# Kernel tuning notes

Measured on AMD Instinct MI355X. Metric: run time of the kernel, lower is better.

## Reference

```python
import jax, jax.numpy as jnp
import numpy as np

NUM_EMBEDDINGS = 1024
EMBEDDING_DIM = 256


def setup_inputs() -> dict:
    key = jax.random.key(0)
    k1, k2 = jax.random.split(key)
    z = jax.random.normal(k1, (32, EMBEDDING_DIM, 32, 32), dtype=jnp.float32)
    codebook = jax.random.normal(k2, (NUM_EMBEDDINGS, EMBEDDING_DIM), dtype=jnp.float32)
    return {"z": z, "codebook": codebook}


def reference(z, codebook):
    # z: (B, C, H, W) -> (B, H, W, C) -> (B*H*W, C)
    B, C, H, W = z.shape
    z_bhwc = jnp.transpose(z, (0, 2, 3, 1))
    z_flat = z_bhwc.reshape(-1, C)  # (N, C)

    # pairwise squared distances: ||z||^2 + ||e||^2 - 2 z.e^T  -> (N, K)
    distances = (
        jnp.sum(z_flat ** 2, axis=1, keepdims=True)
        + jnp.sum(codebook ** 2, axis=1)
        - 2.0 * jnp.matmul(z_flat, codebook.T)
    )
    argmin_codewords = jnp.argmin(distances, axis=1)  # (N,)
    min_codewords = jax.nn.one_hot(argmin_codewords, NUM_EMBEDDINGS, dtype=jnp.float32)  # (N, K)

    # quantized latents via one-hot @ codebook, back to (B, C, H, W)
    z_quantized = jnp.matmul(min_codewords, codebook).reshape(B, H, W, C)
    z_quantized = jnp.transpose(z_quantized, (0, 3, 1, 2))
    return (min_codewords, z_quantized)
```

## Files before the change

kernel.cpp:

```cpp
#include <hip/hip_runtime.h>

#define N_ROWS 32768
#define K_CODES 1024
#define CDIM 256

typedef _Float16 half8 __attribute__((ext_vector_type(8)));
typedef _Float16 half4 __attribute__((ext_vector_type(4)));
typedef float floatx16 __attribute__((ext_vector_type(16)));
typedef unsigned long long ull;

#define WS_ZH   0ull
#define WS_ZL   16777216ull
#define WS_CBH  33554432ull
#define WS_CBL  34078720ull
#define WS_CBN  34603008ull
#define WS_PART 34607104ull
#define WS_IDX  36704256ull
#define WS_NEED 36835328ull

__device__ __forceinline__ void g2lds16(const void* g, void* l) {
    __builtin_amdgcn_global_load_lds(
        (const __attribute__((address_space(1))) void*)g,
        (__attribute__((address_space(3))) void*)l, 16, 0, 0);
}

__global__ __launch_bounds__(256) void prep_all(const float* __restrict__ z,
                                                const float* __restrict__ cb,
                                                _Float16* __restrict__ zh,
                                                _Float16* __restrict__ zl,
                                                _Float16* __restrict__ cbh,
                                                _Float16* __restrict__ cbl,
                                                float* __restrict__ cbn) {
    __shared__ float t[64][68];
    if (blockIdx.x >= 2048) {
        int k = ((blockIdx.x - 2048) << 2) | (threadIdx.x >> 6);
        int lane = threadIdx.x & 63;
        float4 v = reinterpret_cast<const float4*>(cb + k * CDIM)[lane];
        float s0 = v.x * 32.f, s1 = v.y * 32.f, s2 = v.z * 32.f, s3 = v.w * 32.f;
        half4 hv, lv;
        hv[0] = (_Float16)s0; lv[0] = (_Float16)(s0 - (float)hv[0]);
        hv[1] = (_Float16)s1; lv[1] = (_Float16)(s1 - (float)hv[1]);
        hv[2] = (_Float16)s2; lv[2] = (_Float16)(s2 - (float)hv[2]);
        hv[3] = (_Float16)s3; lv[3] = (_Float16)(s3 - (float)hv[3]);
        size_t off = (size_t)((lane >> 3) * K_CODES + k) * 32 + ((lane * 4) & 31);
        *reinterpret_cast<half4*>(&cbh[off]) = hv;
        *reinterpret_cast<half4*>(&cbl[off]) = lv;
        float s = s0 * s0 + s1 * s1 + s2 * s2 + s3 * s3;
        #pragma unroll
        for (int off2 = 32; off2 > 0; off2 >>= 1) s += __shfl_down(s, off2);
        if (lane == 0) cbn[k] = s;
        return;
    }
    int hwt = blockIdx.x & 15;
    int ct  = (blockIdx.x >> 4) & 3;
    int bb  = blockIdx.x >> 6;
    int tid = threadIdx.x;
    #pragma unroll
    for (int p = 0; p < 4; p++) {
        int e = p * 256 + tid;
        int c = e >> 4, h4 = e & 15;
        float4 v = *reinterpret_cast<const float4*>(
            &z[((bb * 256 + ct * 64 + c) << 10) + hwt * 64 + h4 * 4]);
        *reinterpret_cast<float4*>(&t[c][h4 * 4]) = v;
    }
    __syncthreads();
    #pragma unroll
    for (int p = 0; p < 4; p++) {
        int e = p * 256 + tid;
        int hw = e >> 4, c4 = e & 15;
        half4 hv, lv;
        #pragma unroll
        for (int j = 0; j < 4; j++) {
            float s = t[c4 * 4 + j][hw] * 32.f;
            _Float16 h = (_Float16)s;
            hv[j] = h;
            lv[j] = (_Float16)(s - (float)h);
        }
        int n = bb * 1024 + hwt * 64 + hw;
        int cg = ct * 64 + c4 * 4;
        size_t off = (size_t)((cg >> 5) * N_ROWS + n) * 32 + (cg & 31);
        *reinterpret_cast<half4*>(&zh[off]) = hv;
        *reinterpret_cast<half4*>(&zl[off]) = lv;
    }
}

__global__ __launch_bounds__(256, 2) void vq_mfma32(
    const _Float16* __restrict__ zh, const _Float16* __restrict__ zl,
    const _Float16* __restrict__ cbh, const _Float16* __restrict__ cbl,
    const float* __restrict__ cbn, ull* __restrict__ partial) {

    __shared__ _Float16 AhL[2][4096], AlL[2][4096];
    __shared__ _Float16 BhL[2][4096], BlL[2][4096];
    __shared__ float rvv[128][2];
    __shared__ int   rcc[128][2];

    const int tid = threadIdx.x;
    const int lane = tid & 63, wave = tid >> 6;
    const int wm = wave & 1, wn = wave >> 1;
    const int fm = lane & 31, fq = lane >> 5;
    const int codeTile = blockIdx.x & 7;
    const int rowTile  = blockIdx.x >> 3;
    const int rowBase = rowTile * 128, codeBase = codeTile * 128;

    floatx16 acc[4];
    #pragma unroll
    for (int i = 0; i < 4; i++) acc[i] = (floatx16)0.f;

    auto stage = [&](int buf, int ch) {
        const size_t ab = (size_t)(ch * N_ROWS + rowBase) * 32;
        const size_t bbo = (size_t)(ch * K_CODES + codeBase) * 32;
        #pragma unroll
        for (int i = 0; i < 2; i++) {
            int G = i * 256 + tid;
            int q = G >> 7, r = G & 127;
            size_t so = (size_t)r * 32 + q * 8;
            g2lds16(zh + ab + so,  &AhL[buf][G * 8]);
            g2lds16(zl + ab + so,  &AlL[buf][G * 8]);
            g2lds16(cbh + bbo + so, &BhL[buf][G * 8]);
            g2lds16(cbl + bbo + so, &BlL[buf][G * 8]);
        }
    };

    stage(0, 0);
    for (int c = 0; c < 8; c++) {
        const int cur = c & 1;
        if (c < 7) {
            stage(cur ^ 1, c + 1);
            asm volatile("s_waitcnt vmcnt(8)" ::: "memory");
        } else {
            asm volatile("s_waitcnt vmcnt(0)" ::: "memory");
        }
        __builtin_amdgcn_s_barrier();
        #pragma unroll
        for (int s = 0; s < 2; s++) {
            int q = s * 2 + fq;
            half8 ah[2], al[2], bh[2], bl[2];
            #pragma unroll
            for (int i = 0; i < 2; i++) {
                int ga = q * 128 + wm * 64 + i * 32 + fm;
                ah[i] = *reinterpret_cast<const half8*>(&AhL[cur][ga * 8]);
                al[i] = *reinterpret_cast<const half8*>(&AlL[cur][ga * 8]);
            }
            #pragma unroll
            for (int j = 0; j < 2; j++) {
                int gb = q * 128 + wn * 64 + j * 32 + fm;
                bh[j] = *reinterpret_cast<const half8*>(&BhL[cur][gb * 8]);
                bl[j] = *reinterpret_cast<const half8*>(&BlL[cur][gb * 8]);
            }
            #pragma unroll
            for (int i = 0; i < 2; i++)
                #pragma unroll
                for (int j = 0; j < 2; j++) {
                    acc[i*2+j] = __builtin_amdgcn_mfma_f32_32x32x16_f16(ah[i], bh[j], acc[i*2+j], 0, 0, 0);
                    acc[i*2+j] = __builtin_amdgcn_mfma_f32_32x32x16_f16(al[i], bh[j], acc[i*2+j], 0, 0, 0);
                    acc[i*2+j] = __builtin_amdgcn_mfma_f32_32x32x16_f16(ah[i], bl[j], acc[i*2+j], 0, 0, 0);
                }
        }
        __builtin_amdgcn_s_barrier();
    }

    float cbnv[2];
    #pragma unroll
    for (int j = 0; j < 2; j++) cbnv[j] = cbn[codeBase + wn * 64 + j * 32 + fm];

    #pragma unroll
    for (int i = 0; i < 2; i++)
        #pragma unroll
        for (int r = 0; r < 16; r++) {
            float best = 3.4e38f; int bcode = 0x7fffffff;
            #pragma unroll
            for (int j = 0; j < 2; j++) {
                float d = fmaf(-2.f, acc[i*2+j][r], cbnv[j]);
                int code = codeBase + wn * 64 + j * 32 + fm;
                if (d < best) { best = d; bcode = code; }
            }
            #pragma unroll
            for (int m = 1; m < 32; m <<= 1) {
                float ov = __shfl_xor(best, m, 64);
                int   oc = __shfl_xor(bcode, m, 64);
                if (ov < best || (ov == best && oc < bcode)) { best = ov; bcode = oc; }
            }
            if (fm == 0) {
                int row = wm * 64 + i * 32 + (r & 3) + 8 * (r >> 2) + 4 * fq;
                rvv[row][wn] = best;
                rcc[row][wn] = bcode;
            }
        }
    __syncthreads();
    if (tid < 128) {
        float v0 = rvv[tid][0]; int c0 = rcc[tid][0];
        float v1 = rvv[tid][1]; int c1 = rcc[tid][1];
        if (v1 < v0 || (v1 == v0 && c1 < c0)) { v0 = v1; c0 = c1; }
        unsigned u = __float_as_uint(v0);
        u = (u & 0x80000000u) ? ~u : (u | 0x80000000u);
        partial[(size_t)(rowBase + tid) * 8 + codeTile] =
            ((ull)u << 32) | (unsigned)c0;
    }
}

__global__ __launch_bounds__(256) void onehot_fin2(const ull* __restrict__ partial,
                                                   int* __restrict__ idx,
                                                   float* __restrict__ out) {
    __shared__ int sid[16];
    const int rb = blockIdx.x * 16;
    const int tid = threadIdx.x;
    if (tid < 128) {
        ull v = partial[(size_t)rb * 8 + tid];
        #pragma unroll
        for (int m = 1; m < 8; m <<= 1) {
            ull o = __shfl_xor(v, m, 64);
            if (o < v) v = o;
        }
        if ((tid & 7) == 0) {
            int r = tid >> 3;
            int id = (int)(v & 0xffffffffu);
            sid[r] = id;
            idx[rb + r] = id;
        }
    }
    __syncthreads();
    const int k4 = tid << 2;
    #pragma unroll
    for (int r = 0; r < 16; r++) {
        int id = sid[r];
        float4 v4;
        v4.x = (k4     == id) ? 1.f : 0.f;
        v4.y = (k4 + 1 == id) ? 1.f : 0.f;
        v4.z = (k4 + 2 == id) ? 1.f : 0.f;
        v4.w = (k4 + 3 == id) ? 1.f : 0.f;
        reinterpret_cast<float4*>(out)[(size_t)(rb + r) * 256 + tid] = v4;
    }
}

__global__ __launch_bounds__(256) void zq_fill2(const int* __restrict__ idx,
                                                const float* __restrict__ cb,
                                                float* __restrict__ out) {
    __shared__ float tile[64][257];
    const int tid = threadIdx.x;
    const int n0 = (blockIdx.x >> 2) << 8;
    const int c0 = (blockIdx.x & 3) << 6;
    const int b  = n0 >> 10;
    const int hw0 = n0 & 1023;

    const int id = idx[n0 + tid];
    const float4* cb4 = reinterpret_cast<const float4*>(cb);
    #pragma unroll
    for (int jj = 0; jj < 16; jj++) {
        float4 v = cb4[id * 64 + (c0 >> 2) + jj];
        tile[jj * 4 + 0][tid] = v.x;
        tile[jj * 4 + 1][tid] = v.y;
        tile[jj * 4 + 2][tid] = v.z;
        tile[jj * 4 + 3][tid] = v.w;
    }
    __syncthreads();
    #pragma unroll
    for (int c = 0; c < 64; c++) {
        out[((size_t)(b * 256 + c0 + c) << 10) + hw0 + tid] = tile[c][tid];
    }
}


__global__ __launch_bounds__(64) void cb_norms(const float* __restrict__ cb,
                                               float* __restrict__ cbn) {
    int k = blockIdx.x;
    int lane = threadIdx.x;
    float4 v = reinterpret_cast<const float4*>(cb + k * CDIM)[lane];
    float s = v.x * v.x + v.y * v.y + v.z * v.z + v.w * v.w;
    #pragma unroll
    for (int off = 32; off > 0; off >>= 1) s += __shfl_down(s, off);
    if (lane == 0) cbn[k] = s;
}

__global__ __launch_bounds__(256) void cb_transpose(const float* __restrict__ cb,
                                                    float* __restrict__ cbt) {
    __shared__ float t[32][33];
    int k0 = (blockIdx.x & 31) * 32;
    int c0 = (blockIdx.x >> 5) * 32;
    int lane = threadIdx.x & 31;
    int row = threadIdx.x >> 5;
    #pragma unroll
    for (int s = 0; s < 4; s++) {
        int r = row + s * 8;
        t[r][lane] = cb[(k0 + r) * CDIM + c0 + lane];
    }
    __syncthreads();
    #pragma unroll
    for (int s = 0; s < 4; s++) {
        int r = row + s * 8;
        cbt[(c0 + r) * K_CODES + k0 + lane] = t[lane][r];
    }
}

__global__ __launch_bounds__(512, 2) void vq_argmin(const float* __restrict__ z,
                                                    const float* __restrict__ cbt,
                                                    const float* __restrict__ cbn,
                                                    int* __restrict__ idx_out) {
    __shared__ float As[64][128];
    __shared__ float Bs[64][256];

    const int tid = threadIdx.x;
    const int tx = tid & 31;
    const int ty = tid >> 5;
    const int rowBase = blockIdx.x * 128;
    const int bb = rowBase >> 10;
    const int hwBase = rowBase & 1023;

    float minv[8];
    int   mini[8];
    #pragma unroll
    for (int i = 0; i < 8; i++) { minv[i] = 3.4e38f; mini[i] = 0; }

    for (int kt = 0; kt < K_CODES; kt += 256) {
        float acc[2][2][4][4];
        #pragma unroll
        for (int a = 0; a < 2; a++)
            #pragma unroll
            for (int b = 0; b < 2; b++)
                #pragma unroll
                for (int i = 0; i < 4; i++)
                    #pragma unroll
                    for (int j = 0; j < 4; j++) acc[a][b][i][j] = 0.f;

        for (int ccb = 0; ccb < CDIM; ccb += 64) {
            #pragma unroll
            for (int l = 0; l < 4; l++) {
                int f = tid + l * 512;
                int r4 = f & 31, c = f >> 5;
                float4 v = *reinterpret_cast<const float4*>(
                    &z[((bb * 256 + ccb + c) << 10) + hwBase + r4 * 4]);
                *reinterpret_cast<float4*>(&As[c][r4 * 4]) = v;
            }
            #pragma unroll
            for (int l = 0; l < 8; l++) {
                int f = tid + l * 512;
                int k4 = f & 63, c = f >> 6;
                float4 v = *reinterpret_cast<const float4*>(
                    &cbt[(ccb + c) * K_CODES + kt + k4 * 4]);
                *reinterpret_cast<float4*>(&Bs[c][k4 * 4]) = v;
            }
            __syncthreads();
            #pragma unroll 4
            for (int c = 0; c < 64; c++) {
                float4 a0 = *reinterpret_cast<const float4*>(&As[c][ty * 4]);
                float4 a1 = *reinterpret_cast<const float4*>(&As[c][64 + ty * 4]);
                float4 b0 = *reinterpret_cast<const float4*>(&Bs[c][tx * 4]);
                float4 b1 = *reinterpret_cast<const float4*>(&Bs[c][128 + tx * 4]);
                float av[2][4] = {{a0.x, a0.y, a0.z, a0.w}, {a1.x, a1.y, a1.z, a1.w}};
                float bw[2][4] = {{b0.x, b0.y, b0.z, b0.w}, {b1.x, b1.y, b1.z, b1.w}};
                #pragma unroll
                for (int ri = 0; ri < 2; ri++)
                    #pragma unroll
                    for (int i = 0; i < 4; i++)
                        #pragma unroll
                        for (int ci = 0; ci < 2; ci++)
                            #pragma unroll
                            for (int j = 0; j < 4; j++)
                                acc[ri][ci][i][j] =
                                    fmaf(av[ri][i], bw[ci][j], acc[ri][ci][i][j]);
            }
            __syncthreads();
        }
        #pragma unroll
        for (int ci = 0; ci < 2; ci++)
            #pragma unroll
            for (int j = 0; j < 4; j++) {
                int code = kt + ci * 128 + tx * 4 + j;
                float nrm = cbn[code];
                #pragma unroll
                for (int ri = 0; ri < 2; ri++)
                    #pragma unroll
                    for (int i = 0; i < 4; i++) {
                        float d = fmaf(-2.f, acc[ri][ci][i][j], nrm);
                        int r = ri * 4 + i;
                        if (d < minv[r]) { minv[r] = d; mini[r] = code; }
                    }
            }
    }

    __syncthreads();
    float (*rv)[32] = reinterpret_cast<float(*)[32]>(&As[0][0]);
    int   (*rix)[32] = reinterpret_cast<int(*)[32]>(&As[32][0]);
    #pragma unroll
    for (int ri = 0; ri < 2; ri++)
        #pragma unroll
        for (int i = 0; i < 4; i++) {
            int row = ri * 64 + ty * 4 + i;
            rv[row][tx] = minv[ri * 4 + i];
            rix[row][tx] = mini[ri * 4 + i];
        }
    __syncthreads();
    if (tid < 128) {
        float bvv = rv[tid][0]; int bii = rix[tid][0];
        #pragma unroll
        for (int t = 1; t < 32; t++) {
            float v = rv[tid][t]; int ii = rix[tid][t];
            if (v < bvv || (v == bvv && ii < bii)) { bvv = v; bii = ii; }
        }
        idx_out[rowBase + tid] = bii;
    }
}

__global__ __launch_bounds__(256) void onehot_fill(const int* __restrict__ idx,
                                                   float* __restrict__ out) {
    int i = blockIdx.x * 256 + threadIdx.x;
    int n  = i >> 8;
    int k4 = (i & 255) << 2;
    int id = idx[n];
    float4 v;
    v.x = (k4     == id) ? 1.f : 0.f;
    v.y = (k4 + 1 == id) ? 1.f : 0.f;
    v.z = (k4 + 2 == id) ? 1.f : 0.f;
    v.w = (k4 + 3 == id) ? 1.f : 0.f;
    reinterpret_cast<float4*>(out)[i] = v;
}

extern "C" void kernel_launch(void* const* d_in, const int* in_sizes, int n_in,
                              void* d_out, int out_size, void* d_ws, size_t ws_size,
                              hipStream_t stream) {
    const float* z  = (const float*)d_in[0];
    const float* cb = (const float*)d_in[1];
    float* out0 = (float*)d_out;
    float* out1 = out0 + (size_t)N_ROWS * K_CODES;

    if (ws_size >= WS_NEED) {
        _Float16* zh  = (_Float16*)((char*)d_ws + WS_ZH);
        _Float16* zl  = (_Float16*)((char*)d_ws + WS_ZL);
        _Float16* cbh = (_Float16*)((char*)d_ws + WS_CBH);
        _Float16* cbl = (_Float16*)((char*)d_ws + WS_CBL);
        float* cbn = (float*)((char*)d_ws + WS_CBN);
        ull* part = (ull*)((char*)d_ws + WS_PART);
        int* idx = (int*)((char*)d_ws + WS_IDX);

        prep_all<<<2304, 256, 0, stream>>>(z, cb, zh, zl, cbh, cbl, cbn);
        vq_mfma32<<<2048, 256, 0, stream>>>(zh, zl, cbh, cbl, cbn, part);
        onehot_fin2<<<2048, 256, 0, stream>>>(part, idx, out0);
        zq_fill2<<<512, 256, 0, stream>>>(idx, cb, out1);
    } else {
        float* cbn = (float*)d_ws;
        int*   idx = (int*)((char*)d_ws + 4096);
        float* cbt = (float*)((char*)d_ws + 4096 + 131072);

        cb_norms<<<K_CODES, 64, 0, stream>>>(cb, cbn);
        cb_transpose<<<256, 256, 0, stream>>>(cb, cbt);
        vq_argmin<<<N_ROWS / 128, 512, 0, stream>>>(z, cbt, cbn, idx);
        onehot_fill<<<(N_ROWS * K_CODES / 4) / 256, 256, 0, stream>>>(idx, out0);
        zq_fill2<<<512, 256, 0, stream>>>(idx, cb, out1);
    }
}
```

Measured before the change: 313.1 us.

## Single-buffer LDS staging, raise occupancy, reorder tiles, and change chunk layout

Replaces the double-buffered LDS pipeline with a single buffer loaded and synchronised each K-chunk, which halves LDS use and allows launch_bounds to request 4 blocks per SIMD instead of 2. The prep kernel now writes z and codebook in 8-wide half chunks instead of 32-wide, so each 16-byte load reads one contiguous row segment. Block indices are remapped so consecutive blocks share a code tile rather than a row tile. This trades explicit load/compute overlap within a block for overlap across more resident blocks, and it may also cost register pressure.

```diff
diff --git a/kernel.cpp b/kernel.cpp
--- a/kernel.cpp
+++ b/kernel.cpp
@@ -42,7 +42,7 @@
         hv[1] = (_Float16)s1; lv[1] = (_Float16)(s1 - (float)hv[1]);
         hv[2] = (_Float16)s2; lv[2] = (_Float16)(s2 - (float)hv[2]);
         hv[3] = (_Float16)s3; lv[3] = (_Float16)(s3 - (float)hv[3]);
-        size_t off = (size_t)((lane >> 3) * K_CODES + k) * 32 + ((lane * 4) & 31);
+        size_t off = (size_t)((lane >> 1) * K_CODES + k) * 8 + ((lane & 1) * 4);
         *reinterpret_cast<half4*>(&cbh[off]) = hv;
         *reinterpret_cast<half4*>(&cbl[off]) = lv;
         float s = s0 * s0 + s1 * s1 + s2 * s2 + s3 * s3;
@@ -78,19 +78,18 @@
         }
         int n = bb * 1024 + hwt * 64 + hw;
         int cg = ct * 64 + c4 * 4;
-        size_t off = (size_t)((cg >> 5) * N_ROWS + n) * 32 + (cg & 31);
+        size_t off = (size_t)((cg >> 3) * N_ROWS + n) * 8 + (cg & 7);
         *reinterpret_cast<half4*>(&zh[off]) = hv;
         *reinterpret_cast<half4*>(&zl[off]) = lv;
     }
 }
 
-__global__ __launch_bounds__(256, 2) void vq_mfma32(
+__global__ __launch_bounds__(256, 4) void vq_mfma32(
     const _Float16* __restrict__ zh, const _Float16* __restrict__ zl,
     const _Float16* __restrict__ cbh, const _Float16* __restrict__ cbl,
     const float* __restrict__ cbn, ull* __restrict__ partial) {
 
-    __shared__ _Float16 AhL[2][4096], AlL[2][4096];
-    __shared__ _Float16 BhL[2][4096], BlL[2][4096];
+    __shared__ _Float16 AhL[4096], AlL[4096], BhL[4096], BlL[4096];
     __shared__ float rvv[128][2];
     __shared__ int   rcc[128][2];
 
@@ -98,39 +97,28 @@
     const int lane = tid & 63, wave = tid >> 6;
     const int wm = wave & 1, wn = wave >> 1;
     const int fm = lane & 31, fq = lane >> 5;
-    const int codeTile = blockIdx.x & 7;
-    const int rowTile  = blockIdx.x >> 3;
+    const int L = (blockIdx.x & 7) * 256 + (blockIdx.x >> 3);
+    const int codeTile = L & 7;
+    const int rowTile  = L >> 3;
     const int rowBase = rowTile * 128, codeBase = codeTile * 128;
 
     floatx16 acc[4];
     #pragma unroll
     for (int i = 0; i < 4; i++) acc[i] = (floatx16)0.f;
 
-    auto stage = [&](int buf, int ch) {
-        const size_t ab = (size_t)(ch * N_ROWS + rowBase) * 32;
-        const size_t bbo = (size_t)(ch * K_CODES + codeBase) * 32;
+    for (int cc = 0; cc < 8; cc++) {
         #pragma unroll
         for (int i = 0; i < 2; i++) {
             int G = i * 256 + tid;
             int q = G >> 7, r = G & 127;
-            size_t so = (size_t)r * 32 + q * 8;
-            g2lds16(zh + ab + so,  &AhL[buf][G * 8]);
-            g2lds16(zl + ab + so,  &AlL[buf][G * 8]);
-            g2lds16(cbh + bbo + so, &BhL[buf][G * 8]);
-            g2lds16(cbl + bbo + so, &BlL[buf][G * 8]);
-        }
-    };
-
-    stage(0, 0);
-    for (int c = 0; c < 8; c++) {
-        const int cur = c & 1;
-        if (c < 7) {
-            stage(cur ^ 1, c + 1);
-            asm volatile("s_waitcnt vmcnt(8)" ::: "memory");
-        } else {
-            asm volatile("s_waitcnt vmcnt(0)" ::: "memory");
-        }
-        __builtin_amdgcn_s_barrier();
+            size_t ao = ((size_t)(cc * 4 + q) * N_ROWS + rowBase + r) * 8;
+            size_t bo = ((size_t)(cc * 4 + q) * K_CODES + codeBase + r) * 8;
+            g2lds16(zh + ao,  &AhL[G * 8]);
+            g2lds16(zl + ao,  &AlL[G * 8]);
+            g2lds16(cbh + bo, &BhL[G * 8]);
+            g2lds16(cbl + bo, &BlL[G * 8]);
+        }
+        __syncthreads();
         #pragma unroll
         for (int s = 0; s < 2; s++) {
             int q = s * 2 + fq;
@@ -138,14 +126,14 @@
             #pragma unroll
             for (int i = 0; i < 2; i++) {
                 int ga = q * 128 + wm * 64 + i * 32 + fm;
-                ah[i] = *reinterpret_cast<const half8*>(&AhL[cur][ga * 8]);
-                al[i] = *reinterpret_cast<const half8*>(&AlL[cur][ga * 8]);
+                ah[i] = *reinterpret_cast<const half8*>(&AhL[ga * 8]);
+                al[i] = *reinterpret_cast<const half8*>(&AlL[ga * 8]);
             }
             #pragma unroll
             for (int j = 0; j < 2; j++) {
                 int gb = q * 128 + wn * 64 + j * 32 + fm;
-                bh[j] = *reinterpret_cast<const half8*>(&BhL[cur][gb * 8]);
-                bl[j] = *reinterpret_cast<const half8*>(&BlL[cur][gb * 8]);
+                bh[j] = *reinterpret_cast<const half8*>(&BhL[gb * 8]);
+                bl[j] = *reinterpret_cast<const half8*>(&BlL[gb * 8]);
             }
             #pragma unroll
             for (int i = 0; i < 2; i++)
@@ -156,7 +144,7 @@
                     acc[i*2+j] = __builtin_amdgcn_mfma_f32_32x32x16_f16(ah[i], bl[j], acc[i*2+j], 0, 0, 0);
                 }
         }
-        __builtin_amdgcn_s_barrier();
+        __syncthreads();
     }
 
     float cbnv[2];
```

Measured after the change: 279.5 us. 1.12x faster.
